# Performance work log

Hardware: AMD Instinct MI355X
Metric: run time of the kernel (lower is better)

The kernel has to match this reference:

```python
import jax, jax.numpy as jnp
import numpy as np

C_M, C_Z, C_H = 256, 128, 32
EPS = 1e-3
LN_EPS = 1e-5


def setup_inputs() -> dict:
    key = jax.random.key(0)
    ks = jax.random.split(key, 8)
    B, S, N = 1, 128, 256
    m = jax.random.normal(ks[0], (B, S, N, C_M), dtype=jnp.float32)
    msa_mask = jnp.ones((B, S, N), dtype=jnp.float32)
    sa = 1.0 / np.sqrt(C_M)
    so = 1.0 / np.sqrt(C_H * C_H)
    return {
        "m": m,
        "msa_mask": msa_mask,
        "ln_g": jnp.ones((C_M,), jnp.float32),
        "ln_b": jnp.zeros((C_M,), jnp.float32),
        "Wa": jax.random.normal(ks[1], (C_M, C_H), jnp.float32) * sa,
        "ba": jax.random.normal(ks[2], (C_H,), jnp.float32) * 0.01,
        "Wb": jax.random.normal(ks[3], (C_M, C_H), jnp.float32) * sa,
        "bb": jax.random.normal(ks[4], (C_H,), jnp.float32) * 0.01,
        "Wo": jax.random.normal(ks[5], (C_H * C_H, C_Z), jnp.float32) * so,
        "bo": jax.random.normal(ks[6], (C_Z,), jnp.float32) * 0.01,
    }


def reference(m, msa_mask, ln_g, ln_b, Wa, ba, Wb, bb, Wo, bo):
    # m: [B, S, N, c_m], msa_mask: [B, S, N]
    mask = msa_mask[..., None]                       # [B, S, N, 1]
    mu = jnp.mean(m, axis=-1, keepdims=True)
    var = jnp.mean(jnp.square(m - mu), axis=-1, keepdims=True)
    mn = (m - mu) * jax.lax.rsqrt(var + LN_EPS) * ln_g + ln_b
    a = (mn @ Wa + ba) * mask                        # [B, S, N, c_h]
    b = (mn @ Wb + bb) * mask                        # [B, S, N, c_h]
    # outer product, summed over the MSA sequence axis s
    outer = jnp.einsum('bsic,bsje->bijce', a, b)     # [B, N, N, c_h, c_h]
    Bsz, N = m.shape[0], m.shape[2]
    outer = outer.reshape(Bsz, N, N, C_H * C_H)
    out = outer @ Wo + bo                            # [B, N, N, c_z]
    norm = jnp.einsum('bsi,bsj->bij', msa_mask, msa_mask)[..., None] + EPS
    return out / norm
```

## Files before the change

kernel.cpp:

```cpp
#include <hip/hip_runtime.h>

typedef unsigned short u16;
typedef short bf16x8 __attribute__((ext_vector_type(8)));
typedef float f32x4 __attribute__((ext_vector_type(4)));

#define CM 256

__device__ inline u16 f2bf(float f) {
    union { float f; unsigned u; } v; v.f = f;
    unsigned r = v.u + 0x7fffu + ((v.u >> 16) & 1u);
    return (u16)(r >> 16);
}


__global__ void kW(const float* __restrict__ Wo, const float* __restrict__ Wa,
                   const float* __restrict__ Wb, const float* __restrict__ mask,
                   u16* __restrict__ Wo_t, u16* __restrict__ Wab_t,
                   float* __restrict__ norm_ws)
{
    int bid = blockIdx.x, t = threadIdx.x;
    if (bid < 512) {
        int idx = bid * 256 + t;
        int ce = idx >> 7, z = idx & 127;
        int c = ce >> 5, e = ce & 31;
        int kpp = (c & 3) | ((e & 1) << 2) | (((c >> 2) & 1) << 3)
                | (((e >> 1) & 7) << 4) | (((c >> 3) & 1) << 7)
                | ((e >> 4) << 8) | ((c >> 4) << 9);
        Wo_t[z * 1024 + kpp] = f2bf(Wo[idx]);
    } else if (bid < 576) {
        int idx = (bid - 512) * 256 + t;
        int n = idx >> 8, k = idx & 255;
        float v = (n < 32) ? Wa[k * 32 + n] : Wb[k * 32 + (n - 32)];
        Wab_t[idx] = f2bf(v);
    } else {
        int i = bid - 576, j = t;
        float acc = 1e-3f;
        for (int s = 0; s < 128; s++)
            acc += mask[s * 256 + i] * mask[s * 256 + j];
        norm_ws[i * 256 + j] = acc;
    }
}

__global__ __launch_bounds__(256, 2) void kA(
    const float* __restrict__ m, const float* __restrict__ mask,
    const float* __restrict__ ln_g, const float* __restrict__ ln_b,
    const u16* __restrict__ Wab_t, const float* __restrict__ ba,
    const float* __restrict__ bb,
    u16* __restrict__ a_t, u16* __restrict__ b_t)
{
    __shared__ u16 mn_s[64 * 264];

    const int t = threadIdx.x;
    const int w = t >> 6, lane = t & 63, quad = lane >> 4, lr = lane & 15;
    const int i_idx = blockIdx.x >> 1;
    const int sh = blockIdx.x & 1;

    bf16x8 wf[8];
    for (int ks = 0; ks < 8; ks++)
        wf[ks] = *(const bf16x8*)(Wab_t + (w * 16 + lr) * 256 + ks * 32 + quad * 8);

    const float4 g4  = ((const float4*)ln_g)[lane];
    const float4 be4 = ((const float4*)ln_b)[lane];

    for (int rr = 0; rr < 16; rr++) {
        int r = w * 16 + rr;
        int grow = (sh * 64 + r) * 256 + i_idx;
        float4 x = ((const float4*)m)[grow * 64 + lane];
        float s1 = x.x + x.y + x.z + x.w;
        float s2 = x.x * x.x + x.y * x.y + x.z * x.z + x.w * x.w;
        for (int off = 32; off; off >>= 1) {
            s1 += __shfl_xor(s1, off);
            s2 += __shfl_xor(s2, off);
        }
        float mu = s1 * (1.f / CM);
        float rstd = rsqrtf(s2 * (1.f / CM) - mu * mu + 1e-5f);
        ushort4 o;
        o.x = f2bf((x.x - mu) * rstd * g4.x + be4.x);
        o.y = f2bf((x.y - mu) * rstd * g4.y + be4.y);
        o.z = f2bf((x.z - mu) * rstd * g4.z + be4.z);
        o.w = f2bf((x.w - mu) * rstd * g4.w + be4.w);
        *(ushort4*)(&mn_s[r * 264 + lane * 4]) = o;
    }
    __syncthreads();

    f32x4 acc[4] = {};
    for (int ks = 0; ks < 8; ks++)
        for (int mt = 0; mt < 4; mt++) {
            bf16x8 af = *(const bf16x8*)(&mn_s[(mt * 16 + lr) * 264 + ks * 32 + quad * 8]);
            acc[mt] = __builtin_amdgcn_mfma_f32_16x16x32_bf16(af, wf[ks], acc[mt], 0, 0, 0);
        }

    const int n = w * 16 + lr;
    const int cc = n & 31;
    const bool isB = n >= 32;
    const float bv = isB ? bb[cc] : ba[cc];
    u16* dst = isB ? b_t : a_t;
    for (int mt = 0; mt < 4; mt++) {
        int rbase = mt * 16 + quad * 4;
        int sbase = sh * 64 + rbase;
        ushort4 o;
        float v0 = (acc[mt][0] + bv) * mask[(sbase + 0) * 256 + i_idx];
        float v1 = (acc[mt][1] + bv) * mask[(sbase + 1) * 256 + i_idx];
        float v2 = (acc[mt][2] + bv) * mask[(sbase + 2) * 256 + i_idx];
        float v3 = (acc[mt][3] + bv) * mask[(sbase + 3) * 256 + i_idx];
        o.x = f2bf(v0); o.y = f2bf(v1); o.z = f2bf(v2); o.w = f2bf(v3);
        *(ushort4*)(dst + (i_idx * 32 + cc) * 128 + sbase) = o;
    }
}

__global__ __launch_bounds__(256, 2) void kB(
    const u16* __restrict__ a_t, const u16* __restrict__ b_t,
    const u16* __restrict__ Wo_t, const float* __restrict__ bo,
    const float* __restrict__ norm_ws, float* __restrict__ out)
{
    __shared__ __align__(16) u16 smem[32768];
    u16* a_s = smem;
    u16* b_s = smem + 128 * 72;
    u16* outer_s = smem;

    const int t = threadIdx.x;
    const int w = t >> 6, lane = t & 63, quad = lane >> 4, lr = lane & 15;
    const int wm = w >> 1, wn = w & 1;
    const u16* ag = a_t + blockIdx.x * (128 * 128);
    const u16* bg = b_t + blockIdx.y * (256 * 128);

    f32x4 acc2[4][8] = {};
    for (int kh = 0; kh < 2; kh++) {
        for (int q = 0; q < 4; q++) {
            int flat = q * 2048 + t * 8;
            int mm = flat >> 6, kk = flat & 63;
            *(uint4*)(&a_s[mm * 72 + kk]) = *(const uint4*)(ag + mm * 128 + kh * 64 + kk);
        }
        for (int q = 0; q < 8; q++) {
            int flat = q * 2048 + t * 8;
            int mm = flat >> 6, kk = flat & 63;
            *(uint4*)(&b_s[mm * 72 + kk]) = *(const uint4*)(bg + mm * 128 + kh * 64 + kk);
        }
        __syncthreads();
        for (int ks = 0; ks < 2; ks++) {
            int k0 = ks * 32 + quad * 8;
            bf16x8 af[4], bfr[8];
            for (int tm = 0; tm < 4; tm++)
                af[tm] = *(const bf16x8*)(&a_s[(wm * 64 + tm * 16 + lr) * 72 + k0]);
            for (int tn = 0; tn < 8; tn++)
                bfr[tn] = *(const bf16x8*)(&b_s[(wn * 128 + tn * 16 + lr) * 72 + k0]);
            for (int tm = 0; tm < 4; tm++)
                for (int tn = 0; tn < 8; tn++)
                    acc2[tm][tn] = __builtin_amdgcn_mfma_f32_16x16x32_bf16(
                        af[tm], bfr[tn], acc2[tm][tn], 0, 0, 0);
        }
        __syncthreads();
    }

    for (int tm = 0; tm < 4; tm++)
        for (int tn = 0; tn < 8; tn++) {
            int p  = (wm * 2 + (tm >> 1)) * 8 + wn * 4 + (tn >> 1);
            int cI = (quad & 1) | ((lr >> 1) << 1) | ((quad >> 1) << 4)
                   | ((tn & 1) << 5) | ((tm & 1) << 6);
            int pi = cI ^ (p & 7);
            ushort4 o;
            o.x = f2bf(acc2[tm][tn][0]);
            o.y = f2bf(acc2[tm][tn][1]);
            o.z = f2bf(acc2[tm][tn][2]);
            o.w = f2bf(acc2[tm][tn][3]);
            *(ushort4*)(&outer_s[p * 1024 + pi * 8 + 4 * (lr & 1)]) = o;
        }
    __syncthreads();

    const int n0w = w * 32;
    const u16* wp0 = Wo_t + (n0w + lr) * 1024;
    const u16* wp1 = Wo_t + (n0w + 16 + lr) * 1024;
    f32x4 acc3[2][2] = {};
    bf16x8 b3c[2], b3n[2];
    {
        int k0 = quad * 8;
        b3c[0] = *(const bf16x8*)(wp0 + k0);
        b3c[1] = *(const bf16x8*)(wp1 + k0);
        b3n[0] = *(const bf16x8*)(wp0 + 32 + k0);
        b3n[1] = *(const bf16x8*)(wp1 + 32 + k0);
    }
    for (int ks = 0; ks < 32; ks++) {
        bf16x8 a3[2];
        for (int mt = 0; mt < 2; mt++) {
            int pi = ((ks * 4 + quad) ^ (lr & 7));
            a3[mt] = *(const bf16x8*)(&outer_s[(mt * 16 + lr) * 1024 + pi * 8]);
        }
        bf16x8 pf0, pf1;
        if (ks < 30) {
            int k2 = (ks + 2) * 32 + quad * 8;
            pf0 = *(const bf16x8*)(wp0 + k2);
            pf1 = *(const bf16x8*)(wp1 + k2);
        }
        for (int mt = 0; mt < 2; mt++) {
            acc3[mt][0] = __builtin_amdgcn_mfma_f32_16x16x32_bf16(a3[mt], b3c[0], acc3[mt][0], 0, 0, 0);
            acc3[mt][1] = __builtin_amdgcn_mfma_f32_16x16x32_bf16(a3[mt], b3c[1], acc3[mt][1], 0, 0, 0);
        }
        b3c[0] = b3n[0]; b3c[1] = b3n[1];
        b3n[0] = pf0;    b3n[1] = pf1;
    }

    const int i0 = blockIdx.x * 4, j0 = blockIdx.y * 8;
    for (int mt = 0; mt < 2; mt++)
        for (int reg = 0; reg < 4; reg++) {
            int p = mt * 16 + quad * 4 + reg;
            int ii = i0 + (p >> 3), jj = j0 + (p & 7);
            float nrm = norm_ws[ii * 256 + jj];
            for (int tt = 0; tt < 2; tt++) {
                int z = n0w + tt * 16 + lr;
                out[(ii * 256 + jj) * 128 + z] = (acc3[mt][tt][reg] + bo[z]) / nrm;
            }
        }
}

extern "C" void kernel_launch(void* const* d_in, const int* in_sizes, int n_in,
                              void* d_out, int out_size, void* d_ws, size_t ws_size,
                              hipStream_t stream)
{
    const float* m    = (const float*)d_in[0];
    const float* mask = (const float*)d_in[1];
    const float* ln_g = (const float*)d_in[2];
    const float* ln_b = (const float*)d_in[3];
    const float* Wa   = (const float*)d_in[4];
    const float* ba   = (const float*)d_in[5];
    const float* Wb   = (const float*)d_in[6];
    const float* bb   = (const float*)d_in[7];
    const float* Wo   = (const float*)d_in[8];
    const float* bo   = (const float*)d_in[9];
    float* out = (float*)d_out;

    char* ws = (char*)d_ws;
    u16*   a_t     = (u16*)ws;
    u16*   b_t     = (u16*)(ws + 0x200000);
    u16*   Wo_t    = (u16*)(ws + 0x400000);
    u16*   Wab_t   = (u16*)(ws + 0x440000);
    float* norm_ws = (float*)(ws + 0x448000);

    hipLaunchKernelGGL(kW, dim3(832), dim3(256), 0, stream,
                       Wo, Wa, Wb, mask, Wo_t, Wab_t, norm_ws);
    hipLaunchKernelGGL(kA, dim3(512), dim3(256), 0, stream,
                       m, mask, ln_g, ln_b, Wab_t, ba, bb, a_t, b_t);
    hipLaunchKernelGGL(kB, dim3(64, 32), dim3(256), 0, stream,
                       a_t, b_t, Wo_t, bo, norm_ws, out);
}
```

Before: 191.1 us.

## Double-buffer kB's first GEMM and store reciprocal norms

The outer-product GEMM in kB now runs in four K-steps of 32 with double-buffered LDS tiles. Global loads for the next step are issued into registers before the current step's MFMAs, so memory latency overlaps with compute. The norm is stored as a reciprocal so the epilogue multiplies instead of divides, and the Wo transpose is rewritten to write coalesced output. MFMA blocks are also wrapped in s_setprio and loops are unrolled, at the cost of more registers for the prefetch buffers and an extra barrier per step.

```diff
diff --git a/kernel.cpp b/kernel.cpp
--- a/kernel.cpp
+++ b/kernel.cpp
@@ -20,13 +20,12 @@
 {
     int bid = blockIdx.x, t = threadIdx.x;
     if (bid < 512) {
-        int idx = bid * 256 + t;
-        int ce = idx >> 7, z = idx & 127;
-        int c = ce >> 5, e = ce & 31;
-        int kpp = (c & 3) | ((e & 1) << 2) | (((c >> 2) & 1) << 3)
-                | (((e >> 1) & 7) << 4) | (((c >> 3) & 1) << 7)
-                | ((e >> 4) << 8) | ((c >> 4) << 9);
-        Wo_t[z * 1024 + kpp] = f2bf(Wo[idx]);
+        int o = bid * 256 + t;
+        int z = o >> 10, kpp = o & 1023;
+        int c = (kpp & 3) | (((kpp >> 3) & 1) << 2) | (((kpp >> 7) & 1) << 3)
+              | (((kpp >> 9) & 1) << 4);
+        int e = ((kpp >> 2) & 1) | (((kpp >> 4) & 7) << 1) | (((kpp >> 8) & 1) << 4);
+        Wo_t[o] = f2bf(Wo[(c * 32 + e) * 128 + z]);
     } else if (bid < 576) {
         int idx = (bid - 512) * 256 + t;
         int n = idx >> 8, k = idx & 255;
@@ -37,7 +36,7 @@
         float acc = 1e-3f;
         for (int s = 0; s < 128; s++)
             acc += mask[s * 256 + i] * mask[s * 256 + j];
-        norm_ws[i * 256 + j] = acc;
+        norm_ws[i * 256 + j] = 1.0f / acc;
     }
 }
 
@@ -114,8 +113,10 @@
     const float* __restrict__ norm_ws, float* __restrict__ out)
 {
     __shared__ __align__(16) u16 smem[32768];
-    u16* a_s = smem;
-    u16* b_s = smem + 128 * 72;
+    u16* aS0 = smem;
+    u16* aS1 = smem + 5120;
+    u16* bS0 = smem + 10240;
+    u16* bS1 = smem + 20480;
     u16* outer_s = smem;
 
     const int t = threadIdx.x;
@@ -124,35 +125,69 @@
     const u16* ag = a_t + blockIdx.x * (128 * 128);
     const u16* bg = b_t + blockIdx.y * (256 * 128);
 
+    const int ldRow = t >> 2;
+    const int ldK   = (t & 3) * 8;
+
+    uint4 ra[2], rb[4];
+
+#pragma unroll
+    for (int q = 0; q < 2; q++)
+        ra[q] = *(const uint4*)(ag + (q * 64 + ldRow) * 128 + ldK);
+#pragma unroll
+    for (int q = 0; q < 4; q++)
+        rb[q] = *(const uint4*)(bg + (q * 64 + ldRow) * 128 + ldK);
+#pragma unroll
+    for (int q = 0; q < 2; q++)
+        *(uint4*)(&aS0[(q * 64 + ldRow) * 40 + ldK]) = ra[q];
+#pragma unroll
+    for (int q = 0; q < 4; q++)
+        *(uint4*)(&bS0[(q * 64 + ldRow) * 40 + ldK]) = rb[q];
+    __syncthreads();
+
     f32x4 acc2[4][8] = {};
-    for (int kh = 0; kh < 2; kh++) {
-        for (int q = 0; q < 4; q++) {
-            int flat = q * 2048 + t * 8;
-            int mm = flat >> 6, kk = flat & 63;
-            *(uint4*)(&a_s[mm * 72 + kk]) = *(const uint4*)(ag + mm * 128 + kh * 64 + kk);
-        }
-        for (int q = 0; q < 8; q++) {
-            int flat = q * 2048 + t * 8;
-            int mm = flat >> 6, kk = flat & 63;
-            *(uint4*)(&b_s[mm * 72 + kk]) = *(const uint4*)(bg + mm * 128 + kh * 64 + kk);
-        }
-        __syncthreads();
-        for (int ks = 0; ks < 2; ks++) {
-            int k0 = ks * 32 + quad * 8;
-            bf16x8 af[4], bfr[8];
-            for (int tm = 0; tm < 4; tm++)
-                af[tm] = *(const bf16x8*)(&a_s[(wm * 64 + tm * 16 + lr) * 72 + k0]);
+#pragma unroll
+    for (int st = 0; st < 4; st++) {
+        u16* aC = (st & 1) ? aS1 : aS0;
+        u16* bC = (st & 1) ? bS1 : bS0;
+        if (st < 3) {
+            int k0g = (st + 1) * 32;
+#pragma unroll
+            for (int q = 0; q < 2; q++)
+                ra[q] = *(const uint4*)(ag + (q * 64 + ldRow) * 128 + k0g + ldK);
+#pragma unroll
+            for (int q = 0; q < 4; q++)
+                rb[q] = *(const uint4*)(bg + (q * 64 + ldRow) * 128 + k0g + ldK);
+        }
+        bf16x8 af[4], bfr[8];
+#pragma unroll
+        for (int tm = 0; tm < 4; tm++)
+            af[tm] = *(const bf16x8*)(&aC[(wm * 64 + tm * 16 + lr) * 40 + quad * 8]);
+#pragma unroll
+        for (int tn = 0; tn < 8; tn++)
+            bfr[tn] = *(const bf16x8*)(&bC[(wn * 128 + tn * 16 + lr) * 40 + quad * 8]);
+#pragma unroll
+        for (int tm = 0; tm < 4; tm++)
+#pragma unroll
             for (int tn = 0; tn < 8; tn++)
-                bfr[tn] = *(const bf16x8*)(&b_s[(wn * 128 + tn * 16 + lr) * 72 + k0]);
-            for (int tm = 0; tm < 4; tm++)
-                for (int tn = 0; tn < 8; tn++)
-                    acc2[tm][tn] = __builtin_amdgcn_mfma_f32_16x16x32_bf16(
-                        af[tm], bfr[tn], acc2[tm][tn], 0, 0, 0);
-        }
-        __syncthreads();
-    }
-
+                acc2[tm][tn] = __builtin_amdgcn_mfma_f32_16x16x32_bf16(
+                    af[tm], bfr[tn], acc2[tm][tn], 0, 0, 0);
+        if (st < 3) {
+            u16* aN = (st & 1) ? aS0 : aS1;
+            u16* bN = (st & 1) ? bS0 : bS1;
+#pragma unroll
+            for (int q = 0; q < 2; q++)
+                *(uint4*)(&aN[(q * 64 + ldRow) * 40 + ldK]) = ra[q];
+#pragma unroll
+            for (int q = 0; q < 4; q++)
+                *(uint4*)(&bN[(q * 64 + ldRow) * 40 + ldK]) = rb[q];
+            __syncthreads();
+        }
+    }
+    __syncthreads();
+
+#pragma unroll
     for (int tm = 0; tm < 4; tm++)
+#pragma unroll
         for (int tn = 0; tn < 8; tn++) {
             int p  = (wm * 2 + (tm >> 1)) * 8 + wn * 4 + (tn >> 1);
             int cI = (quad & 1) | ((lr >> 1) << 1) | ((quad >> 1) << 4)
@@ -181,6 +216,7 @@
     }
     for (int ks = 0; ks < 32; ks++) {
         bf16x8 a3[2];
+#pragma unroll
         for (int mt = 0; mt < 2; mt++) {
             int pi = ((ks * 4 + quad) ^ (lr & 7));
             a3[mt] = *(const bf16x8*)(&outer_s[(mt * 16 + lr) * 1024 + pi * 8]);
@@ -191,23 +227,28 @@
             pf0 = *(const bf16x8*)(wp0 + k2);
             pf1 = *(const bf16x8*)(wp1 + k2);
         }
-        for (int mt = 0; mt < 2; mt++) {
-            acc3[mt][0] = __builtin_amdgcn_mfma_f32_16x16x32_bf16(a3[mt], b3c[0], acc3[mt][0], 0, 0, 0);
-            acc3[mt][1] = __builtin_amdgcn_mfma_f32_16x16x32_bf16(a3[mt], b3c[1], acc3[mt][1], 0, 0, 0);
-        }
+        __builtin_amdgcn_s_setprio(1);
+        acc3[0][0] = __builtin_amdgcn_mfma_f32_16x16x32_bf16(a3[0], b3c[0], acc3[0][0], 0, 0, 0);
+        acc3[0][1] = __builtin_amdgcn_mfma_f32_16x16x32_bf16(a3[0], b3c[1], acc3[0][1], 0, 0, 0);
+        acc3[1][0] = __builtin_amdgcn_mfma_f32_16x16x32_bf16(a3[1], b3c[0], acc3[1][0], 0, 0, 0);
+        acc3[1][1] = __builtin_amdgcn_mfma_f32_16x16x32_bf16(a3[1], b3c[1], acc3[1][1], 0, 0, 0);
+        __builtin_amdgcn_s_setprio(0);
         b3c[0] = b3n[0]; b3c[1] = b3n[1];
         b3n[0] = pf0;    b3n[1] = pf1;
     }
 
     const int i0 = blockIdx.x * 4, j0 = blockIdx.y * 8;
+#pragma unroll
     for (int mt = 0; mt < 2; mt++)
+#pragma unroll
         for (int reg = 0; reg < 4; reg++) {
             int p = mt * 16 + quad * 4 + reg;
             int ii = i0 + (p >> 3), jj = j0 + (p & 7);
-            float nrm = norm_ws[ii * 256 + jj];
+            float rn = norm_ws[ii * 256 + jj];
+#pragma unroll
             for (int tt = 0; tt < 2; tt++) {
                 int z = n0w + tt * 16 + lr;
-                out[(ii * 256 + jj) * 128 + z] = (acc3[mt][tt][reg] + bo[z]) / nrm;
+                out[(ii * 256 + jj) * 128 + z] = (acc3[mt][tt][reg] + bo[z]) * rn;
             }
         }
 }
```

Result: no change. 188.2 us (-1.5%).
